# Kernel optimization log

Hardware: AMD Instinct MI355X
Metric: run time of the kernel (lower is better)

The kernel has to match this reference:

```python
import jax, jax.numpy as jnp
import numpy as np
import math

N, DS, DV, R, B = 65536, 256, 64, 64, 8
H = DV  # GVP hidden vector channels = max(vi, vo)
EPS = 1e-8
SCALE = 1.0 / math.sqrt(DS + 3 * DV)  # d_total = scalar_dim + 3*vector_dim


def _gvp(s, v, wh, ws_w, ws_b, wv, wsv_w, wsv_b):
    # full GVP with vector_gate=True, activations=(silu, sigmoid)
    vt = jnp.swapaxes(v, -1, -2)                                  # [N, 3, DV]
    vh = vt @ wh.T                                                # [N, 3, H]
    vn = jnp.sqrt(jnp.clip(jnp.sum(vh * vh, axis=-2), EPS))       # [N, H] norm_no_nan
    s_out = jnp.concatenate([s, vn], axis=-1) @ ws_w.T + ws_b     # [N, DS]
    v_out = jnp.swapaxes(vh @ wv.T, -1, -2)                       # [N, DV, 3]
    gate = jax.nn.sigmoid(s_out) @ wsv_w.T + wsv_b                # vector_act(s) then wsv
    v_out = v_out * jax.nn.sigmoid(gate)[..., None]
    return jax.nn.silu(s_out), v_out


def _gvp_scalar(s, v, wh, ws_w, ws_b):
    # gate_gvp: vo=0, activations=(None, None) -> scalar output only
    vt = jnp.swapaxes(v, -1, -2)
    vh = vt @ wh.T
    vn = jnp.sqrt(jnp.clip(jnp.sum(vh * vh, axis=-2), EPS))
    return jnp.concatenate([s, vn], axis=-1) @ ws_w.T + ws_b


def _layernorm(x, g, b):
    mu = x.mean(-1, keepdims=True)
    var = ((x - mu) ** 2).mean(-1, keepdims=True)
    return (x - mu) / jnp.sqrt(var + 1e-5) * g + b


def setup_inputs() -> dict:
    key = jax.random.key(0)
    ks = jax.random.split(key, 32)

    def lin(k, fo, fi):
        return (jax.random.normal(k, (fo, fi), jnp.float32) / np.sqrt(fi)).astype(jnp.float32)

    inp = {
        'x_s': jax.random.normal(ks[0], (N, DS), jnp.float32),
        'x_v': jax.random.normal(ks[1], (N, DV, 3), jnp.float32),
        'batch_index': jnp.sort(jax.random.randint(ks[2], (N,), 0, B, jnp.int32)),
    }
    i = 3
    for name in ('q', 'k', 'v', 'o'):
        inp[f'{name}_wh'] = lin(ks[i], H, DV)
        inp[f'{name}_ws_w'] = lin(ks[i + 1], DS, DS + H)
        inp[f'{name}_ws_b'] = jnp.zeros((DS,), jnp.float32)
        inp[f'{name}_wv'] = lin(ks[i + 2], DV, H)
        inp[f'{name}_wsv_w'] = lin(ks[i + 3], DV, DS)
        inp[f'{name}_wsv_b'] = jnp.zeros((DV,), jnp.float32)
        i += 4
    inp['comp_w1'] = lin(ks[i], DS, DS)
    inp['comp_b1'] = jnp.zeros((DS,), jnp.float32)
    inp['ln_g'] = jnp.ones((DS,), jnp.float32)
    inp['ln_b'] = jnp.zeros((DS,), jnp.float32)
    inp['comp_w2'] = lin(ks[i + 1], R, DS)
    inp['comp_b2'] = jnp.zeros((R,), jnp.float32)
    inp['g_wh'] = lin(ks[i + 2], H, DV)
    inp['g_ws_w'] = lin(ks[i + 3], DS, DS + H)
    inp['g_ws_b'] = jnp.zeros((DS,), jnp.float32)
    inp['gate_bias'] = jnp.full((DS,), -1.0, jnp.float32)
    return inp


def reference(x_s, x_v, batch_index,
              q_wh, q_ws_w, q_ws_b, q_wv, q_wsv_w, q_wsv_b,
              k_wh, k_ws_w, k_ws_b, k_wv, k_wsv_w, k_wsv_b,
              v_wh, v_ws_w, v_ws_b, v_wv, v_wsv_w, v_wsv_b,
              o_wh, o_ws_w, o_ws_b, o_wv, o_wsv_w, o_wsv_b,
              comp_w1, comp_b1, ln_g, ln_b, comp_w2, comp_b2,
              g_wh, g_ws_w, g_ws_b, gate_bias):
    Q_s, Q_v = _gvp(x_s, x_v, q_wh, q_ws_w, q_ws_b, q_wv, q_wsv_w, q_wsv_b)
    K_s, K_v = _gvp(x_s, x_v, k_wh, k_ws_w, k_ws_b, k_wv, k_wsv_w, k_wsv_b)
    V_s, V_v = _gvp(x_s, x_v, v_wh, v_ws_w, v_ws_b, v_wv, v_wsv_w, v_wsv_b)

    h = _layernorm(x_s @ comp_w1.T + comp_b1, ln_g, ln_b)
    P = jax.nn.softmax(jax.nn.silu(h) @ comp_w2.T + comp_b2, axis=-1)  # [N, R]

    out_s = jnp.zeros_like(x_s)
    out_v = jnp.zeros_like(x_v)
    # per-graph anchor compression + retrieval (B is a small fixed graph count)
    for b in range(B):
        m = (batch_index == b).astype(x_s.dtype)                  # [N]
        Pm = P * m[:, None]                                       # masked soft assignment
        Kbs = Pm.T @ K_s                                          # [R, DS]
        Vbs = Pm.T @ V_s                                          # [R, DS]
        Kbv = jnp.einsum('nr,nvc->rvc', Pm, K_v)                  # [R, DV, 3]
        Vbv = jnp.einsum('nr,nvc->rvc', Pm, V_v)                  # [R, DV, 3]
        logits = (Q_s @ Kbs.T + jnp.einsum('nvc,rvc->nr', Q_v, Kbv)) * SCALE
        attn = jax.nn.softmax(logits, axis=-1)                    # [N, R]
        out_s = out_s + m[:, None] * (attn @ Vbs)
        out_v = out_v + m[:, None, None] * jnp.einsum('nr,rvc->nvc', attn, Vbv)

    gate_s = jax.nn.sigmoid(_gvp_scalar(x_s, x_v, g_wh, g_ws_w, g_ws_b) + gate_bias)
    gate_v = jax.nn.sigmoid(gate_s.mean(-1, keepdims=True))[..., None]
    return _gvp(out_s * gate_s, out_v * gate_v,
                o_wh, o_ws_w, o_ws_b, o_wv, o_wsv_w, o_wsv_b)
```

## Files before the change

### kernel.cpp

```cpp
#include <hip/hip_runtime.h>

typedef unsigned short u16;
typedef __attribute__((ext_vector_type(8))) short bs8;
typedef __attribute__((ext_vector_type(4))) short bs4;
typedef __attribute__((ext_vector_type(4))) float fx4;
#define MFMA16(a,b,c) __builtin_amdgcn_mfma_f32_16x16x32_bf16(a,b,c,0,0,0)

__device__ __forceinline__ float b2f(u16 u){ return __uint_as_float(((unsigned int)u) << 16); }
__device__ __forceinline__ u16 f2b(float f){
  unsigned int x = __float_as_uint(f);
  unsigned int r = (x + 0x7FFFu + ((x >> 16) & 1u)) >> 16;
  return (u16)r;
}
__device__ __forceinline__ float rcpf(float x){ return __builtin_amdgcn_rcpf(x); }
__device__ __forceinline__ float sigm(float x){ return rcpf(1.f+__expf(-x)); }
__device__ __forceinline__ float siluf(float x){ return x*rcpf(1.f+__expf(-x)); }
__device__ __forceinline__ float wsum(float v){
  #pragma unroll
  for (int o=1;o<64;o<<=1) v += __shfl_xor(v, o);
  return v;
}
__device__ __forceinline__ float wmax(float v){
  #pragma unroll
  for (int o=1;o<64;o<<=1) v = fmaxf(v, __shfl_xor(v, o));
  return v;
}
__device__ __forceinline__ bs8 lds8(const u16* ptr){ return *reinterpret_cast<const bs8*>(ptr); }
__device__ __forceinline__ bs8 glb8(const u16* ptr){ return *reinterpret_cast<const bs8*>(ptr); }

#define XSB_P 328
#define XVB_P 72
#define SGB_P 264
#define UBUF_P 68
#define XQ_P 456
#define AT_P 72

struct GP {
  const float* x_s; const float* x_v; const int* bidx;
  const float* wh[5]; const float* ws_w[5]; const float* ws_b[5];
  const float* wv[4]; const float* wsv_w[4]; const float* wsv_b[4];
  const float *w1, *b1, *lng, *lnb, *w2, *b2, *gbias;
  u16 *wsP, *whP, *wvP, *wsvP, *w1P, *w2P;
  float *wsb_f, *wsvb_f, *b1_f, *b2_f, *lng_f, *lnb_f, *gb_f;
  u16 *KP, *VP, *Gs, *PT, *QB;
  float *Gv, *CK, *CV;
  u16 *CKP, *CVP;
  int *bstart;
  float *Qs, *Qv;
};

__global__ __launch_bounds__(256) void kprep(GP p){
  int idx = blockIdx.x*256 + threadIdx.x;
  if (idx < 409600){
    int s=idx/81920, r=idx%81920;
    int ks=r/8192, r2=r%8192, nt=r2/512, r3=r2%512, ln=r3/8, j=r3%8;
    int n=nt*16+(ln&15), k=ks*32+((ln>>4)*8)+j;
    p.wsP[idx] = f2b(p.ws_w[s][n*320+k]); return;
  }
  idx -= 409600;
  if (idx < 20480){
    int s=idx/4096, r=idx%4096;
    int ks=r/2048, r2=r%2048, nt=r2/512, r3=r2%512, ln=r3/8, j=r3%8;
    int h=nt*16+(ln&15), d=ks*32+((ln>>4)*8)+j;
    p.whP[idx] = f2b(p.wh[s][h*64+d]); return;
  }
  idx -= 20480;
  if (idx < 16384){
    int s=idx/4096, r=idx%4096;
    int ks=r/2048, r2=r%2048, nt=r2/512, r3=r2%512, ln=r3/8, j=r3%8;
    int dd=nt*16+(ln&15), hh=ks*32+((ln>>4)*8)+j;
    p.wvP[idx] = f2b(p.wv[s][dd*64+hh]); return;
  }
  idx -= 16384;
  if (idx < 65536){
    int s=idx/16384, r=idx%16384;
    int ks=r/2048, r2=r%2048, nt=r2/512, r3=r2%512, ln=r3/8, j=r3%8;
    int dd=nt*16+(ln&15), i=ks*32+((ln>>4)*8)+j;
    p.wsvP[idx] = f2b(p.wsv_w[s][dd*256+i]); return;
  }
  idx -= 65536;
  if (idx < 65536){
    int ks=idx/8192, r2=idx%8192, nt=r2/512, r3=r2%512, ln=r3/8, j=r3%8;
    int n=nt*16+(ln&15), k=ks*32+((ln>>4)*8)+j;
    p.w1P[idx] = f2b(p.w1[n*256+k]); return;
  }
  idx -= 65536;
  if (idx < 16384){
    int ks=idx/2048, r2=idx%2048, nt=r2/512, r3=r2%512, ln=r3/8, j=r3%8;
    int rr=nt*16+(ln&15), i=ks*32+((ln>>4)*8)+j;
    p.w2P[idx] = f2b(p.w2[rr*256+i]); return;
  }
  idx -= 16384;
  if (idx < 1280){ int s=idx>>8, i=idx&255; p.wsb_f[idx] = p.ws_b[s][i]; return; }
  idx -= 1280;
  if (idx < 256){ int s=idx>>6, d=idx&63; p.wsvb_f[idx] = p.wsv_b[s][d]; return; }
  idx -= 256;
  if (idx < 256){ p.b1_f[idx] = p.b1[idx]; return; }
  idx -= 256;
  if (idx < 64){ p.b2_f[idx] = p.b2[idx]; return; }
  idx -= 64;
  if (idx < 256){ p.lng_f[idx] = p.lng[idx]; return; }
  idx -= 256;
  if (idx < 256){ p.lnb_f[idx] = p.lnb[idx]; return; }
  idx -= 256;
  if (idx < 256){ p.gb_f[idx] = p.gbias[idx]; return; }
  idx -= 256;
  if (idx < 65536){
    if (idx == 0){
      int b0 = p.bidx[0];
      for (int b=0;b<=b0;b++) p.bstart[b]=0;
      int bl = p.bidx[65535];
      for (int b=bl+1;b<=8;b++) p.bstart[b]=65536;
    } else {
      int a = p.bidx[idx-1], c = p.bidx[idx];
      for (int b=a+1;b<=c;b++) p.bstart[b] = idx;
    }
    return;
  }
}

__device__ __forceinline__ void mfma_vh_vn(const u16* whPs, const u16* xvb, u16* vhb2,
                                           u16* xsb, int lane, int w4){
  fx4 a0={0,0,0,0}, a1={0,0,0,0}, a2={0,0,0,0};
  #pragma unroll
  for (int ks=0; ks<2; ks++){
    bs8 b = glb8(whPs + (ks*4+w4)*512 + lane*8);
    bs8 x0 = lds8(xvb + ( 0 + (lane&15))*XVB_P + ks*32 + ((lane>>4)*8));
    bs8 x1 = lds8(xvb + (16 + (lane&15))*XVB_P + ks*32 + ((lane>>4)*8));
    bs8 x2 = lds8(xvb + (32 + (lane&15))*XVB_P + ks*32 + ((lane>>4)*8));
    a0 = MFMA16(x0,b,a0); a1 = MFMA16(x1,b,a1); a2 = MFMA16(x2,b,a2);
  }
  int h = w4*16 + (lane&15);
  int mrow = (lane>>4)*4;
  #pragma unroll
  for (int r=0;r<4;r++){
    vhb2[( 0+mrow+r)*XVB_P + h] = f2b(a0[r]);
    vhb2[(16+mrow+r)*XVB_P + h] = f2b(a1[r]);
    vhb2[(32+mrow+r)*XVB_P + h] = f2b(a2[r]);
    float nv = __builtin_amdgcn_sqrtf(
        fmaxf(a0[r]*a0[r] + a1[r]*a1[r] + a2[r]*a2[r], 1e-8f));
    xsb[(mrow+r)*XSB_P + 256 + h] = f2b(nv);
  }
  __syncthreads();
}

template<int KS>
__device__ __forceinline__ void mfma_sgemm(const u16* wsPs, const float* bias,
                                           const u16* xsb, int lane, int w4, fx4 acc[4]){
  #pragma unroll
  for (int t=0;t<4;t++) acc[t] = (fx4){0.f,0.f,0.f,0.f};
  const u16* arow = xsb + (lane&15)*XSB_P + ((lane>>4)*8);
  #pragma unroll
  for (int ks=0; ks<KS; ks++){
    bs8 a = lds8(arow + ks*32);
    #pragma unroll
    for (int t=0;t<4;t++){
      bs8 b = glb8(wsPs + (ks*16 + w4*4 + t)*512 + lane*8);
      acc[t] = MFMA16(a,b,acc[t]);
    }
  }
  #pragma unroll
  for (int t=0;t<4;t++){
    float bv = bias[(w4*4+t)*16 + (lane&15)];
    acc[t][0]+=bv; acc[t][1]+=bv; acc[t][2]+=bv; acc[t][3]+=bv;
  }
}

__device__ __forceinline__ fx4 mfma_g64(const u16* bP, const u16* sgb, int lane, int w4){
  fx4 acc = {0.f,0.f,0.f,0.f};
  const u16* arow = sgb + (lane&15)*SGB_P + ((lane>>4)*8);
  #pragma unroll
  for (int ks=0; ks<8; ks++){
    bs8 a = lds8(arow + ks*32);
    bs8 b = glb8(bP + (ks*4 + w4)*512 + lane*8);
    acc = MFMA16(a,b,acc);
  }
  return acc;
}

__device__ __forceinline__ void mfma_wv(const u16* wvPs, const u16* vhb2,
                                        int lane, int w4, fx4 vo[3]){
  vo[0]=(fx4){0.f,0.f,0.f,0.f}; vo[1]=vo[0]; vo[2]=vo[0];
  #pragma unroll
  for (int ks=0; ks<2; ks++){
    bs8 b = glb8(wvPs + (ks*4+w4)*512 + lane*8);
    #pragma unroll
    for (int c=0;c<3;c++){
      bs8 a = lds8(vhb2 + (c*16 + (lane&15))*XVB_P + ks*32 + ((lane>>4)*8));
      vo[c] = MFMA16(a,b,vo[c]);
    }
  }
}

__global__ __launch_bounds__(512, 4) void k1(GP p){
  __shared__ __align__(16) u16 xsb[32*XSB_P];
  __shared__ __align__(16) u16 xvb[96*XVB_P];
  __shared__ __align__(16) u16 vhb2[96*XVB_P];
  __shared__ __align__(16) u16 sgb[32*SGB_P];
  __shared__ float red[2][8][16];
  __shared__ float lnp[2][2][16];
  __shared__ float ubuf[32*UBUF_P];
  const int tid = threadIdx.x, lane = tid&63, wave = tid>>6;
  const int w4 = wave&3, hv = wave>>2;
  const int ml = lane&15, gl = lane>>4;
  const int n0 = blockIdx.x * 32;
  const int nb = n0 + hv*16;
  u16* xsbH  = xsb  + hv*16*XSB_P;
  u16* xvbH  = xvb  + hv*48*XVB_P;
  u16* vhb2H = vhb2 + hv*48*XVB_P;
  u16* sgbH  = sgb  + hv*16*SGB_P;

  for (int i=tid;i<2048;i+=512){
    int node=i>>6, c4=(i&63)*4;
    float4 v = *reinterpret_cast<const float4*>(p.x_s + (size_t)(n0+node)*256 + c4);
    u16* d = xsb + node*XSB_P + c4;
    d[0]=f2b(v.x); d[1]=f2b(v.y); d[2]=f2b(v.z); d[3]=f2b(v.w);
  }
  for (int i=tid;i<6144;i+=512){
    int row=i>>6, d=i&63;
    int h=row/48, rr=row-48*h, c=rr>>4, nl=rr&15;
    xvb[row*XVB_P+d] = f2b(p.x_v[(size_t)(n0+h*16+nl)*192 + d*3 + c]);
  }
  __syncthreads();

  fx4 acc[4];
  #pragma unroll 1
  for (int s=0; s<3; ++s){
    mfma_vh_vn(p.whP + s*4096, xvbH, vhb2H, xsbH, lane, w4);
    mfma_sgemm<10>(p.wsP + (size_t)s*81920, p.wsb_f + s*256, xsbH, lane, w4, acc);
    #pragma unroll
    for (int t=0;t<4;t++){
      int ncol=(w4*4+t)*16+ml;
      bs4 st;
      #pragma unroll
      for (int r=0;r<4;r++){
        int node=gl*4+r;
        float v=acc[t][r];
        float sg=rcpf(1.f+__expf(-v));
        u16 slb = f2b(v*sg);
        if (s==0) p.QB[(size_t)(nb+node)*448+ncol]=slb;
        else      st[r]=(short)slb;
        sgbH[node*SGB_P+ncol]=f2b(sg);
      }
      if (s!=0){
        u16* KVp = (s==1)? p.KP : p.VP;
        *reinterpret_cast<bs4*>(KVp + ((size_t)((n0>>4)+hv)*448 + ncol)*16 + gl*4) = st;
      }
    }
    __syncthreads();
    fx4 g = mfma_g64(p.wsvP + s*16384, sgbH, lane, w4);
    fx4 vo[3];
    mfma_wv(p.wvP + s*4096, vhb2H, lane, w4, vo);
    int dout = w4*16+ml;
    if (s==0){
      #pragma unroll
      for (int r=0;r<4;r++){
        int node=gl*4+r;
        float gg = sigm(g[r] + p.wsvb_f[dout]);
        #pragma unroll
        for (int c=0;c<3;c++)
          p.QB[(size_t)(nb+node)*448 + 256 + c*64 + dout] = f2b(vo[c][r]*gg);
      }
    } else {
      u16* KVp=(s==1)?p.KP:p.VP;
      float gg[4];
      #pragma unroll
      for (int r=0;r<4;r++) gg[r] = sigm(g[r] + p.wsvb_f[s*64+dout]);
      #pragma unroll
      for (int c=0;c<3;c++){
        bs4 st;
        #pragma unroll
        for (int r=0;r<4;r++) st[r]=(short)f2b(vo[c][r]*gg[r]);
        *reinterpret_cast<bs4*>(KVp + ((size_t)((n0>>4)+hv)*448 + 256 + c*64 + dout)*16 + gl*4) = st;
      }
    }
    __syncthreads();
  }

  mfma_vh_vn(p.whP + 3*4096, xvbH, vhb2H, xsbH, lane, w4);
  mfma_sgemm<10>(p.wsP + (size_t)3*81920, p.wsb_f + 3*256, xsbH, lane, w4, acc);
  {
    float psum[4] = {0.f,0.f,0.f,0.f};
    #pragma unroll
    for (int t=0;t<4;t++){
      int ncol=(w4*4+t)*16+ml;
      float gb = p.gb_f[ncol];
      #pragma unroll
      for (int r=0;r<4;r++){
        int node=gl*4+r;
        float gs = sigm(acc[t][r] + gb);
        p.Gs[(size_t)(nb+node)*256+ncol] = f2b(gs);
        psum[r] += gs;
      }
    }
    #pragma unroll
    for (int r=0;r<4;r++){
      #pragma unroll
      for (int o=1;o<16;o<<=1) psum[r] += __shfl_xor(psum[r], o);
    }
    if (ml==0){
      #pragma unroll
      for (int r=0;r<4;r++) red[hv][w4][gl*4+r] = psum[r];
    }
    __syncthreads();
    if (tid<32){
      int h=tid>>4, nl=tid&15;
      p.Gv[n0+tid] = sigm((red[h][0][nl]+red[h][1][nl]+red[h][2][nl]+red[h][3][nl])*(1.f/256.f));
    }
    __syncthreads();
  }

  mfma_sgemm<8>(p.w1P, p.b1_f, xsbH, lane, w4, acc);
  {
    float s1[4]={0.f,0.f,0.f,0.f}, s2[4]={0.f,0.f,0.f,0.f};
    #pragma unroll
    for (int t=0;t<4;t++)
      #pragma unroll
      for (int r=0;r<4;r++){ float v=acc[t][r]; s1[r]+=v; s2[r]+=v*v; }
    #pragma unroll
    for (int r=0;r<4;r++){
      #pragma unroll
      for (int o=1;o<16;o<<=1){ s1[r]+=__shfl_xor(s1[r],o); s2[r]+=__shfl_xor(s2[r],o); }
    }
    if (ml==0){
      #pragma unroll
      for (int r=0;r<4;r++){
        red[hv][w4][gl*4+r]=s1[r];
        red[hv][4+w4][gl*4+r]=s2[r];
      }
    }
    __syncthreads();
    if (tid<32){
      int h=tid>>4, nl=tid&15;
      float S1=red[h][0][nl]+red[h][1][nl]+red[h][2][nl]+red[h][3][nl];
      float S2=red[h][4][nl]+red[h][5][nl]+red[h][6][nl]+red[h][7][nl];
      float mu=S1*(1.f/256.f), var=S2*(1.f/256.f)-mu*mu;
      lnp[h][0][nl]=mu; lnp[h][1][nl]=rsqrtf(var+1e-5f);
    }
    __syncthreads();
    #pragma unroll
    for (int t=0;t<4;t++){
      int ncol=(w4*4+t)*16+ml;
      float g=p.lng_f[ncol], b=p.lnb_f[ncol];
      #pragma unroll
      for (int r=0;r<4;r++){
        int node=gl*4+r;
        float h=(acc[t][r]-lnp[hv][0][node])*lnp[hv][1][node]*g + b;
        sgbH[node*SGB_P+ncol]=f2b(siluf(h));
      }
    }
    __syncthreads();
    fx4 u = mfma_g64(p.w2P, sgbH, lane, w4);
    int rcol = w4*16+ml;
    float b2v = p.b2_f[rcol];
    #pragma unroll
    for (int r=0;r<4;r++)
      ubuf[(hv*16 + gl*4+r)*UBUF_P + rcol] = u[r] + b2v;
    __syncthreads();
    bs4 pt4;
    #pragma unroll
    for (int i=0;i<4;i++){
      int node = wave*4+i;
      float uu = ubuf[node*UBUF_P + lane];
      float m = wmax(uu);
      float e = __expf(uu-m);
      float ss = wsum(e);
      pt4[i] = (short)f2b(e*rcpf(ss));
    }
    *reinterpret_cast<bs4*>(p.PT + ((size_t)((n0>>4)+(wave>>2))*64 + lane)*16 + (wave&3)*4) = pt4;
  }
}

__device__ __forceinline__ bs8 ldfrag(const u16* base, int n8, int row, int stride){
  return *reinterpret_cast<const bs8*>(base + ((size_t)(n8>>4)*stride + row)*16 + (n8&15));
}

__global__ __launch_bounds__(256) void k2(GP p){
  const int bid = blockIdx.x;
  const int bb = bid >> 5;
  const int sv = (bid >> 4) & 1;
  const int sp = bid & 15;
  const int lane = threadIdx.x & 63, wave = threadIdx.x >> 6;
  const int ml = lane & 15, gl = lane >> 4;
  int s0 = p.bstart[bb], s1 = p.bstart[bb+1];
  int len = s1 - s0; if (len <= 0) return;
  int cl = (((len + 15) >> 4) + 7) & ~7;
  int kb0 = s0 + sp*cl; if (kb0 >= s1) return;
  int kb1 = kb0 + cl; if (kb1 > s1) kb1 = s1;
  int kba = kb0 & ~7;
  const u16* F = sv ? p.VP : p.KP;
  fx4 acc[4][7];
  #pragma unroll
  for (int m=0;m<4;m++)
    #pragma unroll
    for (int t=0;t<7;t++) acc[m][t]=(fx4){0.f,0.f,0.f,0.f};

  for (int kb = kba; kb < kb1; kb += 32){
    int n8 = kb + gl*8;
    bool edge = (kb < kb0) | (kb + 32 > kb1);
    bs8 a[4];
    #pragma unroll
    for (int m=0;m<4;m++) a[m] = ldfrag(p.PT, n8, m*16+ml, 64);
    if (edge){
      #pragma unroll
      for (int j=0;j<8;j++){
        int n = n8 + j;
        if (n < kb0 || n >= kb1){
          #pragma unroll
          for (int m=0;m<4;m++) a[m][j]=0;
        }
      }
    }
    #pragma unroll
    for (int t=0;t<7;t++){
      bs8 bf = ldfrag(F, n8, (wave*7+t)*16+ml, 448);
      if (edge){
        #pragma unroll
        for (int j=0;j<8;j++){
          int n = n8 + j;
          if (n < kb0 || n >= kb1) bf[j]=0;
        }
      }
      #pragma unroll
      for (int m=0;m<4;m++) acc[m][t] = MFMA16(a[m], bf, acc[m][t]);
    }
  }
  #pragma unroll
  for (int m=0;m<4;m++){
    #pragma unroll
    for (int t=0;t<7;t++){
      int f = (wave*7+t)*16 + ml;
      int r0 = m*16 + gl*4;
      if (sv==0){
        float* dst = p.CK + ((size_t)bb*448+f)*64 + r0;
        #pragma unroll
        for (int j=0;j<4;j++) atomicAdd(dst+j, acc[m][t][j]);
      } else {
        float* dst = p.CV + ((size_t)bb*64+r0)*448 + f;
        #pragma unroll
        for (int j=0;j<4;j++) atomicAdd(dst + (size_t)j*448, acc[m][t][j]);
      }
    }
  }
}

__global__ __launch_bounds__(256) void k2b(GP p){
  int idx = blockIdx.x*256 + threadIdx.x;
  if (idx < 229376){
    int b=idx/28672, r=idx%28672;
    int ks=r/2048, r2=r%2048, nt=r2/512, r3=r2%512, ln=r3/8, j=r3&7;
    int f=ks*32+((ln>>4)*8)+j, rr=nt*16+(ln&15);
    p.CKP[idx] = f2b(p.CK[((size_t)b*448+f)*64+rr] * 0.047245559f);
    return;
  }
  idx -= 229376;
  int b=idx/28672, r=idx%28672;
  int ks=r/14336, r2=r%14336, nt=r2/512, r3=r2%512, ln=r3/8, j=r3&7;
  int rr=ks*32+((ln>>4)*8)+j, f=nt*16+(ln&15);
  p.CVP[idx] = f2b(p.CV[((size_t)b*64+rr)*448+f]);
}

__global__ __launch_bounds__(512, 4) void k3(GP p){
  __shared__ __align__(16) char smem[68608];
  u16* xq   = (u16*)smem;
  u16* atb  = (u16*)(smem+29184);
  u16* xsb  = (u16*)(smem+33792);
  u16* xvb  = (u16*)(smem+54784);
  u16* vhb2 = (u16*)smem;
  u16* sgb  = (u16*)(smem+13824);
  __shared__ float redm[2][4][16];
  __shared__ float reds[2][4][16];
  __shared__ int Bl[32];
  const int tid = threadIdx.x;
  const int n0 = blockIdx.x * 32;
  const int lane = tid & 63, wave = tid >> 6;
  const int w4 = wave&3, hv = wave>>2;
  const int ml = lane&15, gl = lane>>4;
  const int nb = n0 + hv*16;
  u16* xqH   = xq   + hv*16*XQ_P;
  u16* atbH  = atb  + hv*16*AT_P;
  u16* xsbH  = xsb  + hv*16*XSB_P;
  u16* xvbH  = xvb  + hv*48*XVB_P;
  u16* vhb2H = vhb2 + hv*48*XVB_P;
  u16* sgbH  = sgb  + hv*16*SGB_P;
  const int* BlH = Bl + hv*16;

  for (int idx=tid; idx<1792; idx+=512){
    int node = idx/56, q = idx-node*56;
    bs8 v = *reinterpret_cast<const bs8*>(p.QB + (size_t)(n0+node)*448 + q*8);
    *reinterpret_cast<bs8*>(xq + node*XQ_P + q*8) = v;
  }
  if (tid<32) Bl[tid] = p.bidx[n0+tid];
  __syncthreads();

  int bb = Bl[0];
  while (true){
    fx4 lac = {0.f,0.f,0.f,0.f};
    {
      const u16* ckb = p.CKP + (size_t)bb*28672;
      const u16* arow = xqH + ml*XQ_P + gl*8;
      #pragma unroll
      for (int ks=0; ks<14; ks++){
        bs8 a = lds8(arow + ks*32);
        bs8 b = glb8(ckb + (ks*4+w4)*512 + lane*8);
        lac = MFMA16(a,b,lac);
      }
    }
    float loc[4];
    #pragma unroll
    for (int r=0;r<4;r++){
      float m = lac[r];
      #pragma unroll
      for (int o=1;o<16;o<<=1) m = fmaxf(m, __shfl_xor(m,o));
      loc[r]=m;
    }
    if (ml==0){
      #pragma unroll
      for (int r=0;r<4;r++) redm[hv][w4][gl*4+r]=loc[r];
    }
    __syncthreads();
    float e4[4];
    #pragma unroll
    for (int r=0;r<4;r++){
      int node=gl*4+r;
      float gm = fmaxf(fmaxf(redm[hv][0][node],redm[hv][1][node]),
                       fmaxf(redm[hv][2][node],redm[hv][3][node]));
      float e = __expf(lac[r]-gm);
      e4[r]=e;
      float s=e;
      #pragma unroll
      for (int o=1;o<16;o<<=1) s += __shfl_xor(s,o);
      loc[r]=s;
    }
    if (ml==0){
      #pragma unroll
      for (int r=0;r<4;r++) reds[hv][w4][gl*4+r]=loc[r];
    }
    __syncthreads();
    #pragma unroll
    for (int r=0;r<4;r++){
      int node=gl*4+r;
      float tot = reds[hv][0][node]+reds[hv][1][node]+reds[hv][2][node]+reds[hv][3][node];
      atbH[node*AT_P + w4*16 + ml] = f2b(e4[r]*rcpf(tot));
    }
    __syncthreads();
    {
      const u16* cvb = p.CVP + (size_t)bb*28672;
      const u16* prow = atbH + ml*AT_P + gl*8;
      bs8 a0 = lds8(prow);
      bs8 a1 = lds8(prow + 32);
      #pragma unroll
      for (int t=0;t<7;t++){
        int nt = w4*7 + t;
        fx4 pv = {0.f,0.f,0.f,0.f};
        pv = MFMA16(a0, glb8(cvb + nt*512 + lane*8), pv);
        pv = MFMA16(a1, glb8(cvb + (28+nt)*512 + lane*8), pv);
        int f = nt*16 + ml;
        #pragma unroll
        for (int r=0;r<4;r++){
          int node=gl*4+r;
          if (BlH[node]!=bb) continue;
          int n = nb+node;
          if (f < 256){
            float gs = b2f(p.Gs[(size_t)n*256+f]);
            xsbH[node*XSB_P+f] = f2b(pv[r]*gs);
          } else {
            int fm=f-256, c=fm>>6, d=fm&63;
            xvbH[(c*16+node)*XVB_P+d] = f2b(pv[r]*p.Gv[n]);
          }
        }
      }
    }
    int nxt = 0x7fffffff;
    #pragma unroll
    for (int i=0;i<32;i++){ int v=Bl[i]; if (v>bb && v<nxt) nxt=v; }
    if (nxt==0x7fffffff) break;
    bb = nxt;
    __syncthreads();
  }
  __syncthreads();

  mfma_vh_vn(p.whP + 4*4096, xvbH, vhb2H, xsbH, lane, w4);
  fx4 acc[4];
  mfma_sgemm<10>(p.wsP + (size_t)4*81920, p.wsb_f + 4*256, xsbH, lane, w4, acc);
  #pragma unroll
  for (int t=0;t<4;t++){
    int ncol=(w4*4+t)*16+ml;
    #pragma unroll
    for (int r=0;r<4;r++){
      int node=gl*4+r;
      float v=acc[t][r];
      float sg=rcpf(1.f+__expf(-v));
      p.Qs[(size_t)(nb+node)*256+ncol]=v*sg;
      sgbH[node*SGB_P+ncol]=f2b(sg);
    }
  }
  __syncthreads();
  fx4 g = mfma_g64(p.wsvP + 3*16384, sgbH, lane, w4);
  fx4 vo[3];
  mfma_wv(p.wvP + 3*4096, vhb2H, lane, w4, vo);
  int dout = w4*16+ml;
  #pragma unroll
  for (int r=0;r<4;r++){
    int node=gl*4+r;
    float gg = sigm(g[r] + p.wsvb_f[3*64+dout]);
    #pragma unroll
    for (int c=0;c<3;c++)
      p.Qv[(size_t)(nb+node)*192 + dout*3 + c] = vo[c][r]*gg;
  }
}

extern "C" void kernel_launch(void* const* d_in, const int* in_sizes, int n_in,
                              void* d_out, int out_size, void* d_ws, size_t ws_size,
                              hipStream_t stream){
  (void)in_sizes; (void)n_in; (void)out_size; (void)ws_size;
  GP p;
  p.x_s  = (const float*)d_in[0];
  p.x_v  = (const float*)d_in[1];
  p.bidx = (const int*)d_in[2];
  const int whI[5]  = {3, 9, 15, 33, 21};
  const int wswI[5] = {4, 10, 16, 34, 22};
  const int wsbI[5] = {5, 11, 17, 35, 23};
  const int wvI[4]  = {6, 12, 18, 24};
  const int wsvwI[4]= {7, 13, 19, 25};
  const int wsvbI[4]= {8, 14, 20, 26};
  for (int s=0;s<5;s++){
    p.wh[s]   = (const float*)d_in[whI[s]];
    p.ws_w[s] = (const float*)d_in[wswI[s]];
    p.ws_b[s] = (const float*)d_in[wsbI[s]];
  }
  for (int s=0;s<4;s++){
    p.wv[s]    = (const float*)d_in[wvI[s]];
    p.wsv_w[s] = (const float*)d_in[wsvwI[s]];
    p.wsv_b[s] = (const float*)d_in[wsvbI[s]];
  }
  p.w1    = (const float*)d_in[27];
  p.b1    = (const float*)d_in[28];
  p.lng   = (const float*)d_in[29];
  p.lnb   = (const float*)d_in[30];
  p.w2    = (const float*)d_in[31];
  p.b2    = (const float*)d_in[32];
  p.gbias = (const float*)d_in[36];

  char* w = (char*)d_ws;
  auto alloc = [&](size_t bytes)->char*{
    char* r = w; w += (bytes + 255) & ~(size_t)255; return r;
  };
  p.wsP   = (u16*)alloc(409600u*2);
  p.whP   = (u16*)alloc(20480u*2);
  p.wvP   = (u16*)alloc(16384u*2);
  p.wsvP  = (u16*)alloc(65536u*2);
  p.w1P   = (u16*)alloc(65536u*2);
  p.w2P   = (u16*)alloc(16384u*2);
  p.wsb_f  = (float*)alloc(1280u*4);
  p.wsvb_f = (float*)alloc(256u*4);
  p.b1_f   = (float*)alloc(256u*4);
  p.b2_f   = (float*)alloc(64u*4);
  p.lng_f  = (float*)alloc(256u*4);
  p.lnb_f  = (float*)alloc(256u*4);
  p.gb_f   = (float*)alloc(256u*4);
  p.QB = (u16*)alloc((size_t)65536*448*2);
  p.KP = (u16*)alloc((size_t)65536*448*2 + (1u<<22));
  p.VP = (u16*)alloc((size_t)65536*448*2 + (1u<<22));
  p.Gs = (u16*)alloc((size_t)65536*256*2);
  p.PT = (u16*)alloc((size_t)65536*64*2 + (1u<<20));
  p.Gv = (float*)alloc((size_t)65536*4);
  p.CK = (float*)alloc((size_t)8*448*64*4);
  p.CV = (float*)alloc((size_t)8*448*64*4);
  p.CKP = (u16*)alloc((size_t)8*448*64*2);
  p.CVP = (u16*)alloc((size_t)8*448*64*2);
  p.bstart = (int*)alloc(64);
  p.Qs = (float*)d_out;
  p.Qv = (float*)d_out + (size_t)65536*256;

  hipMemsetAsync(p.CK, 0, (size_t)8*448*64*4, stream);
  hipMemsetAsync(p.CV, 0, (size_t)8*448*64*4, stream);
  kprep<<<2587, 256, 0, stream>>>(p);
  k1<<<2048, 512, 0, stream>>>(p);
  k2<<<256, 256, 0, stream>>>(p);
  k2b<<<1792, 256, 0, stream>>>(p);
  k3<<<2048, 512, 0, stream>>>(p);
}
```

Baseline: 824.7 us.

## Retile scalar GEMMs so each wave covers both node halves, halving weight loads

The scalar-output MFMA GEMMs are retiled so each of the 8 waves computes 2 column tiles for both 16-node halves, instead of 4 column tiles for one half. Each weight fragment loaded from global memory now feeds two MFMAs, halving global weight traffic per block. The epilogues, reductions and LayerNorm statistics are rewritten for the new ownership, using an extra reduction buffer. Some global stores are moved after the barrier. This costs more LDS A-operand reads and cross-half synchronisation.

```diff
diff --git a/kernel.cpp b/kernel.cpp
--- a/kernel.cpp
+++ b/kernel.cpp
@@ -145,24 +145,31 @@
 }
 
 template<int KS>
-__device__ __forceinline__ void mfma_sgemm(const u16* wsPs, const float* bias,
-                                           const u16* xsb, int lane, int w4, fx4 acc[4]){
-  #pragma unroll
-  for (int t=0;t<4;t++) acc[t] = (fx4){0.f,0.f,0.f,0.f};
-  const u16* arow = xsb + (lane&15)*XSB_P + ((lane>>4)*8);
+__device__ __forceinline__ void mfma_sgemm2(const u16* wsPs, const float* bias,
+                                            const u16* xsb, int lane, int wave,
+                                            fx4 acc[2][2]){
+  #pragma unroll
+  for (int h=0;h<2;h++)
+    #pragma unroll
+    for (int t=0;t<2;t++) acc[h][t]=(fx4){0.f,0.f,0.f,0.f};
+  const u16* arow0 = xsb + (lane&15)*XSB_P + ((lane>>4)*8);
+  const u16* arow1 = arow0 + 16*XSB_P;
   #pragma unroll
   for (int ks=0; ks<KS; ks++){
-    bs8 a = lds8(arow + ks*32);
-    #pragma unroll
-    for (int t=0;t<4;t++){
-      bs8 b = glb8(wsPs + (ks*16 + w4*4 + t)*512 + lane*8);
-      acc[t] = MFMA16(a,b,acc[t]);
-    }
-  }
-  #pragma unroll
-  for (int t=0;t<4;t++){
-    float bv = bias[(w4*4+t)*16 + (lane&15)];
-    acc[t][0]+=bv; acc[t][1]+=bv; acc[t][2]+=bv; acc[t][3]+=bv;
+    bs8 a0 = lds8(arow0 + ks*32);
+    bs8 a1 = lds8(arow1 + ks*32);
+    bs8 b0 = glb8(wsPs + (ks*16 + wave*2+0)*512 + lane*8);
+    bs8 b1 = glb8(wsPs + (ks*16 + wave*2+1)*512 + lane*8);
+    acc[0][0]=MFMA16(a0,b0,acc[0][0]); acc[0][1]=MFMA16(a0,b1,acc[0][1]);
+    acc[1][0]=MFMA16(a1,b0,acc[1][0]); acc[1][1]=MFMA16(a1,b1,acc[1][1]);
+  }
+  #pragma unroll
+  for (int t=0;t<2;t++){
+    float bv = bias[(wave*2+t)*16 + (lane&15)];
+    #pragma unroll
+    for (int h=0;h<2;h++){
+      acc[h][t][0]+=bv; acc[h][t][1]+=bv; acc[h][t][2]+=bv; acc[h][t][3]+=bv;
+    }
   }
 }
 
@@ -198,13 +205,13 @@
   __shared__ __align__(16) u16 vhb2[96*XVB_P];
   __shared__ __align__(16) u16 sgb[32*SGB_P];
   __shared__ float red[2][8][16];
+  __shared__ float redb[2][8][16];
   __shared__ float lnp[2][2][16];
   __shared__ float ubuf[32*UBUF_P];
   const int tid = threadIdx.x, lane = tid&63, wave = tid>>6;
   const int w4 = wave&3, hv = wave>>2;
   const int ml = lane&15, gl = lane>>4;
   const int n0 = blockIdx.x * 32;
-  const int nb = n0 + hv*16;
   u16* xsbH  = xsb  + hv*16*XSB_P;
   u16* xvbH  = xvb  + hv*48*XVB_P;
   u16* vhb2H = vhb2 + hv*48*XVB_P;
@@ -223,35 +230,53 @@
   }
   __syncthreads();
 
-  fx4 acc[4];
+  fx4 acc[2][2];
   #pragma unroll 1
   for (int s=0; s<3; ++s){
     mfma_vh_vn(p.whP + s*4096, xvbH, vhb2H, xsbH, lane, w4);
-    mfma_sgemm<10>(p.wsP + (size_t)s*81920, p.wsb_f + s*256, xsbH, lane, w4, acc);
-    #pragma unroll
-    for (int t=0;t<4;t++){
-      int ncol=(w4*4+t)*16+ml;
-      bs4 st;
-      #pragma unroll
-      for (int r=0;r<4;r++){
-        int node=gl*4+r;
-        float v=acc[t][r];
-        float sg=rcpf(1.f+__expf(-v));
-        u16 slb = f2b(v*sg);
-        if (s==0) p.QB[(size_t)(nb+node)*448+ncol]=slb;
-        else      st[r]=(short)slb;
-        sgbH[node*SGB_P+ncol]=f2b(sg);
-      }
-      if (s!=0){
-        u16* KVp = (s==1)? p.KP : p.VP;
-        *reinterpret_cast<bs4*>(KVp + ((size_t)((n0>>4)+hv)*448 + ncol)*16 + gl*4) = st;
-      }
-    }
-    __syncthreads();
+    mfma_sgemm2<10>(p.wsP + (size_t)s*81920, p.wsb_f + s*256, xsb, lane, wave, acc);
+    bs4 stv[2][2];
+    #pragma unroll
+    for (int h=0;h<2;h++){
+      #pragma unroll
+      for (int t=0;t<2;t++){
+        int ncol=(wave*2+t)*16+ml;
+        #pragma unroll
+        for (int r=0;r<4;r++){
+          int node16=gl*4+r;
+          float v=acc[h][t][r];
+          float sg=rcpf(1.f+__expf(-v));
+          stv[h][t][r]=(short)f2b(v*sg);
+          sgb[(h*16+node16)*SGB_P+ncol]=f2b(sg);
+        }
+      }
+    }
+    __syncthreads();
+    if (s==0){
+      #pragma unroll
+      for (int h=0;h<2;h++)
+        #pragma unroll
+        for (int t=0;t<2;t++){
+          int ncol=(wave*2+t)*16+ml;
+          #pragma unroll
+          for (int r=0;r<4;r++)
+            p.QB[(size_t)(n0+h*16+gl*4+r)*448+ncol]=(u16)stv[h][t][r];
+        }
+    } else {
+      u16* KVp = (s==1)? p.KP : p.VP;
+      #pragma unroll
+      for (int h=0;h<2;h++)
+        #pragma unroll
+        for (int t=0;t<2;t++){
+          int ncol=(wave*2+t)*16+ml;
+          *reinterpret_cast<bs4*>(KVp + ((size_t)((n0>>4)+h)*448 + ncol)*16 + gl*4) = stv[h][t];
+        }
+    }
     fx4 g = mfma_g64(p.wsvP + s*16384, sgbH, lane, w4);
     fx4 vo[3];
     mfma_wv(p.wvP + s*4096, vhb2H, lane, w4, vo);
     int dout = w4*16+ml;
+    const int nb = n0 + hv*16;
     if (s==0){
       #pragma unroll
       for (int r=0;r<4;r++){
@@ -278,77 +303,106 @@
   }
 
   mfma_vh_vn(p.whP + 3*4096, xvbH, vhb2H, xsbH, lane, w4);
-  mfma_sgemm<10>(p.wsP + (size_t)3*81920, p.wsb_f + 3*256, xsbH, lane, w4, acc);
+  mfma_sgemm2<10>(p.wsP + (size_t)3*81920, p.wsb_f + 3*256, xsb, lane, wave, acc);
   {
-    float psum[4] = {0.f,0.f,0.f,0.f};
-    #pragma unroll
-    for (int t=0;t<4;t++){
-      int ncol=(w4*4+t)*16+ml;
-      float gb = p.gb_f[ncol];
+    float psum[2][4] = {{0.f,0.f,0.f,0.f},{0.f,0.f,0.f,0.f}};
+    u16 gsv[2][2][4];
+    #pragma unroll
+    for (int h=0;h<2;h++){
+      #pragma unroll
+      for (int t=0;t<2;t++){
+        int ncol=(wave*2+t)*16+ml;
+        float gb = p.gb_f[ncol];
+        #pragma unroll
+        for (int r=0;r<4;r++){
+          float gs = sigm(acc[h][t][r] + gb);
+          gsv[h][t][r]=f2b(gs);
+          psum[h][r] += gs;
+        }
+      }
+    }
+    #pragma unroll
+    for (int h=0;h<2;h++)
       #pragma unroll
       for (int r=0;r<4;r++){
-        int node=gl*4+r;
-        float gs = sigm(acc[t][r] + gb);
-        p.Gs[(size_t)(nb+node)*256+ncol] = f2b(gs);
-        psum[r] += gs;
-      }
-    }
-    #pragma unroll
-    for (int r=0;r<4;r++){
-      #pragma unroll
-      for (int o=1;o<16;o<<=1) psum[r] += __shfl_xor(psum[r], o);
-    }
+        #pragma unroll
+        for (int o=1;o<16;o<<=1) psum[h][r] += __shfl_xor(psum[h][r], o);
+      }
     if (ml==0){
       #pragma unroll
-      for (int r=0;r<4;r++) red[hv][w4][gl*4+r] = psum[r];
-    }
-    __syncthreads();
+      for (int h=0;h<2;h++)
+        #pragma unroll
+        for (int r=0;r<4;r++) red[h][wave][gl*4+r] = psum[h][r];
+    }
+    __syncthreads();
+    #pragma unroll
+    for (int h=0;h<2;h++)
+      #pragma unroll
+      for (int t=0;t<2;t++){
+        int ncol=(wave*2+t)*16+ml;
+        #pragma unroll
+        for (int r=0;r<4;r++)
+          p.Gs[(size_t)(n0+h*16+gl*4+r)*256+ncol] = gsv[h][t][r];
+      }
     if (tid<32){
       int h=tid>>4, nl=tid&15;
-      p.Gv[n0+tid] = sigm((red[h][0][nl]+red[h][1][nl]+red[h][2][nl]+red[h][3][nl])*(1.f/256.f));
-    }
-    __syncthreads();
-  }
-
-  mfma_sgemm<8>(p.w1P, p.b1_f, xsbH, lane, w4, acc);
+      float s8 = red[h][0][nl]+red[h][1][nl]+red[h][2][nl]+red[h][3][nl]
+               + red[h][4][nl]+red[h][5][nl]+red[h][6][nl]+red[h][7][nl];
+      p.Gv[n0+tid] = sigm(s8*(1.f/256.f));
+    }
+    __syncthreads();
+  }
+
+  mfma_sgemm2<8>(p.w1P, p.b1_f, xsb, lane, wave, acc);
   {
-    float s1[4]={0.f,0.f,0.f,0.f}, s2[4]={0.f,0.f,0.f,0.f};
-    #pragma unroll
-    for (int t=0;t<4;t++)
-      #pragma unroll
-      for (int r=0;r<4;r++){ float v=acc[t][r]; s1[r]+=v; s2[r]+=v*v; }
-    #pragma unroll
-    for (int r=0;r<4;r++){
-      #pragma unroll
-      for (int o=1;o<16;o<<=1){ s1[r]+=__shfl_xor(s1[r],o); s2[r]+=__shfl_xor(s2[r],o); }
-    }
+    float s1[2][4]={{0.f,0.f,0.f,0.f},{0.f,0.f,0.f,0.f}};
+    float s2[2][4]={{0.f,0.f,0.f,0.f},{0.f,0.f,0.f,0.f}};
+    #pragma unroll
+    for (int h=0;h<2;h++)
+      #pragma unroll
+      for (int t=0;t<2;t++)
+        #pragma unroll
+        for (int r=0;r<4;r++){ float v=acc[h][t][r]; s1[h][r]+=v; s2[h][r]+=v*v; }
+    #pragma unroll
+    for (int h=0;h<2;h++)
+      #pragma unroll
+      for (int r=0;r<4;r++){
+        #pragma unroll
+        for (int o=1;o<16;o<<=1){ s1[h][r]+=__shfl_xor(s1[h][r],o); s2[h][r]+=__shfl_xor(s2[h][r],o); }
+      }
     if (ml==0){
       #pragma unroll
-      for (int r=0;r<4;r++){
-        red[hv][w4][gl*4+r]=s1[r];
-        red[hv][4+w4][gl*4+r]=s2[r];
-      }
+      for (int h=0;h<2;h++)
+        #pragma unroll
+        for (int r=0;r<4;r++){
+          red[h][wave][gl*4+r]=s1[h][r];
+          redb[h][wave][gl*4+r]=s2[h][r];
+        }
     }
     __syncthreads();
     if (tid<32){
       int h=tid>>4, nl=tid&15;
-      float S1=red[h][0][nl]+red[h][1][nl]+red[h][2][nl]+red[h][3][nl];
-      float S2=red[h][4][nl]+red[h][5][nl]+red[h][6][nl]+red[h][7][nl];
+      float S1=red[h][0][nl]+red[h][1][nl]+red[h][2][nl]+red[h][3][nl]
+             + red[h][4][nl]+red[h][5][nl]+red[h][6][nl]+red[h][7][nl];
+      float S2=redb[h][0][nl]+redb[h][1][nl]+redb[h][2][nl]+redb[h][3][nl]
+             + redb[h][4][nl]+redb[h][5][nl]+redb[h][6][nl]+redb[h][7][nl];
       float mu=S1*(1.f/256.f), var=S2*(1.f/256.f)-mu*mu;
       lnp[h][0][nl]=mu; lnp[h][1][nl]=rsqrtf(var+1e-5f);
     }
     __syncthreads();
     #pragma unroll
-    for (int t=0;t<4;t++){
-      int ncol=(w4*4+t)*16+ml;
-      float g=p.lng_f[ncol], b=p.lnb_f[ncol];
-      #pragma unroll
-      for (int r=0;r<4;r++){
-        int node=gl*4+r;
-        float h=(acc[t][r]-lnp[hv][0][node])*lnp[hv][1][node]*g + b;
-        sgbH[node*SGB_P+ncol]=f2b(siluf(h));
-      }
-    }
+    for (int h=0;h<2;h++)
+      #pragma unroll
+      for (int t=0;t<2;t++){
+        int ncol=(wave*2+t)*16+ml;
+        float g=p.lng_f[ncol], b=p.lnb_f[ncol];
+        #pragma unroll
+        for (int r=0;r<4;r++){
+          int node16=gl*4+r;
+          float hh=(acc[h][t][r]-lnp[h][0][node16])*lnp[h][1][node16]*g + b;
+          sgb[(h*16+node16)*SGB_P+ncol]=f2b(siluf(hh));
+        }
+      }
     __syncthreads();
     fx4 u = mfma_g64(p.w2P, sgbH, lane, w4);
     int rcol = w4*16+ml;
@@ -581,18 +635,21 @@
   __syncthreads();
 
   mfma_vh_vn(p.whP + 4*4096, xvbH, vhb2H, xsbH, lane, w4);
-  fx4 acc[4];
-  mfma_sgemm<10>(p.wsP + (size_t)4*81920, p.wsb_f + 4*256, xsbH, lane, w4, acc);
-  #pragma unroll
-  for (int t=0;t<4;t++){
-    int ncol=(w4*4+t)*16+ml;
-    #pragma unroll
-    for (int r=0;r<4;r++){
-      int node=gl*4+r;
-      float v=acc[t][r];
-      float sg=rcpf(1.f+__expf(-v));
-      p.Qs[(size_t)(nb+node)*256+ncol]=v*sg;
-      sgbH[node*SGB_P+ncol]=f2b(sg);
+  fx4 acc[2][2];
+  mfma_sgemm2<10>(p.wsP + (size_t)4*81920, p.wsb_f + 4*256, xsb, lane, wave, acc);
+  #pragma unroll
+  for (int h=0;h<2;h++){
+    #pragma unroll
+    for (int t=0;t<2;t++){
+      int ncol=(wave*2+t)*16+ml;
+      #pragma unroll
+      for (int r=0;r<4;r++){
+        int node16=gl*4+r;
+        float v=acc[h][t][r];
+        float sg=rcpf(1.f+__expf(-v));
+        p.Qs[(size_t)(n0+h*16+node16)*256+ncol]=v*sg;
+        sgb[(h*16+node16)*SGB_P+ncol]=f2b(sg);
+      }
     }
   }
   __syncthreads();
```

Measured after the change: 725.8 us. -12.0%, faster.
